# Performance work log

Hardware: AMD Instinct MI355X
Metric: run time of the kernel (lower is better)

Reference implementation:

```python
import jax, jax.numpy as jnp
import numpy as np

B, S, D, H, E, KW = 2, 2048, 1024, 8, 128, 16  # batch, seq, d_model, heads, head_width, kernel_width


def setup_inputs() -> dict:
    key = jax.random.key(0)
    ks = jax.random.split(key, 10)
    sc = D ** -0.5
    x = jax.random.normal(ks[0], (B, S, D), dtype=jnp.float32)
    Wq = jax.random.normal(ks[1], (H, D, E), dtype=jnp.float32) * sc
    bq = jnp.zeros((H, E), dtype=jnp.float32)
    Wk = jax.random.normal(ks[2], (H, D, E), dtype=jnp.float32) * sc
    bk = jnp.zeros((H, E), dtype=jnp.float32)
    Wv = jax.random.normal(ks[3], (H, D, E), dtype=jnp.float32) * sc
    bv = jnp.zeros((H, E), dtype=jnp.float32)
    Wo = jax.random.normal(ks[4], (H, E, D), dtype=jnp.float32) * ((H * E) ** -0.5)
    bo = jnp.zeros((D,), dtype=jnp.float32)
    dilations = jnp.array([1, 1, 2, 2, 4, 4, 8, 8], dtype=jnp.int32)
    return {"x": x, "Wq": Wq, "bq": bq, "Wk": Wk, "bk": bk,
            "Wv": Wv, "bv": bv, "Wo": Wo, "bo": bo, "dilations": dilations}


def _windows(kh, vh, bkh, bvh, d):
    # kh, vh: [B, S, E] projected keys/values for one head; d: dilation (scalar int)
    s = kh.shape[1]
    # center-justified dilated window: positions i + d*j - d*(KW-1)//2
    pos = jnp.arange(s)[:, None] + d * jnp.arange(KW)[None, :] - (d * (KW - 1)) // 2
    valid = (pos >= 0) & (pos < s)            # [S, KW]
    posc = jnp.clip(pos, 0, s - 1)
    # padded positions hold the zero-embedding, whose projection is just the bias
    kw = jnp.where(valid[None, :, :, None], kh[:, posc, :], bkh)  # [B, S, KW, E]
    vw = jnp.where(valid[None, :, :, None], vh[:, posc, :], bvh)
    return kw, vw


def _lcsa(x, Wq, bq, Wk, bk, Wv, bv, Wo, bo, dilations):
    # per-head independent projections (Core.Linear with parallel shape [heads])
    q = jnp.einsum('bsd,hde->bhse', x, Wq) + bq[None, :, None, :]       # [B,H,S,E]
    k_all = jnp.einsum('bsd,hde->bhse', x, Wk) + bk[None, :, None, :]
    v_all = jnp.einsum('bsd,hde->bhse', x, Wv) + bv[None, :, None, :]
    # gather dilated local windows per head (project-then-gather; padded = bias)
    kw, vw = jax.vmap(_windows, in_axes=(1, 1, 0, 0, 0))(k_all, v_all, bk, bv, dilations)
    # kw, vw: [H, B, S, KW, E]
    logits = jnp.einsum('bhse,hbske->bhsk', q, kw)                       # [B,H,S,KW]
    score = jax.nn.softmax(logits, axis=-1)
    # NOTE: original divides by sqrt(d_head) AFTER softmax*value (faithful quirk)
    attn = jnp.einsum('bhsk,hbske->bhse', score, vw) / jnp.sqrt(jnp.asarray(E, x.dtype))
    out = jnp.einsum('bhse,hed->bsd', attn, Wo) + bo                     # dehead merge
    return out


def reference(x, Wq, bq, Wk, bk, Wv, bv, Wo, bo, dilations):
    return _lcsa(x, Wq, bq, Wk, bk, Wv, bv, Wo, bo, dilations)
```

## Files before the change

### kernel.cpp

```cpp
#include <hip/hip_runtime.h>
#include <stdint.h>

#define Bb 2
#define Ss 2048
#define Dd 1024
#define Hh 8
#define Ee 128
#define KWW 16
#define Mm (Bb*Ss)
#define Kk 1024

typedef unsigned short u16;
typedef __attribute__((ext_vector_type(8))) _Float16 f16x8;
typedef __attribute__((ext_vector_type(4))) float f32x4;

__device__ __forceinline__ u16 f2h(float f) {
  union { _Float16 h; u16 u; } v; v.h = (_Float16)f; return v.u;
}
__device__ __forceinline__ float h2f(u16 u) {
  union { u16 u; _Float16 h; } v; v.u = u; return (float)v.h;
}
__device__ __forceinline__ float h2f_lo(uint32_t w) { return h2f((u16)(w & 0xFFFF)); }
__device__ __forceinline__ float h2f_hi(uint32_t w) { return h2f((u16)(w >> 16)); }

__device__ __forceinline__ void gll16(const void* g, void* l) {
  __builtin_amdgcn_global_load_lds((const __attribute__((address_space(1))) void*)g,
                                   (__attribute__((address_space(3))) void*)l, 16, 0, 0);
}

__global__ __launch_bounds__(256) void prep(
    const float* __restrict__ x, const float* __restrict__ Wq,
    const float* __restrict__ Wk, const float* __restrict__ Wv,
    const float* __restrict__ Wo,
    u16* __restrict__ xh, u16* __restrict__ wT, u16* __restrict__ woT) {
  const int bid = blockIdx.x;
  const int tid = threadIdx.x;
  if (bid < 4096) {
    int i = (bid * 256 + tid) * 4;
    float4 f = *(const float4*)(x + i);
    uint64_t pk = (uint64_t)f2h(f.x) | ((uint64_t)f2h(f.y) << 16) |
                  ((uint64_t)f2h(f.z) << 32) | ((uint64_t)f2h(f.w) << 48);
    *(uint64_t*)(xh + i) = pk;
    return;
  }
  __shared__ float tile[32][33];
  const int tx = tid & 31, ty = tid >> 5;
  if (bid < 4096 + 3072) {
    const int idx = bid - 4096;
    const int z = idx >> 7, rem = idx & 127;
    const int h = z & 7;
    const float* W = (z < 8) ? Wq : (z < 16) ? Wk : Wv;
    const float* ib = W + (size_t)h * Dd * Ee;
    u16* ob = wT + (size_t)z * Ee * Kk;
    const int r0 = (rem & 31) * 32, c0 = (rem >> 5) * 32;
    #pragma unroll
    for (int kq = 0; kq < 4; kq++)
      tile[ty + 8*kq][tx] = ib[(size_t)(r0 + ty + 8*kq) * Ee + (c0 + tx)];
    __syncthreads();
    #pragma unroll
    for (int kq = 0; kq < 4; kq++)
      ob[(size_t)(c0 + ty + 8*kq) * Dd + (r0 + tx)] = f2h(tile[tx][ty + 8*kq]);
  } else {
    const int idx = bid - (4096 + 3072);
    const int r0 = (idx & 31) * 32, c0 = (idx >> 5) * 32;
    const int R = Hh * Ee, C = Dd;
    #pragma unroll
    for (int kq = 0; kq < 4; kq++)
      tile[ty + 8*kq][tx] = Wo[(size_t)(r0 + ty + 8*kq) * C + (c0 + tx)];
    __syncthreads();
    #pragma unroll
    for (int kq = 0; kq < 4; kq++)
      woT[(size_t)(c0 + ty + 8*kq) * R + (r0 + tx)] = f2h(tile[tx][ty + 8*kq]);
  }
}

template<int MT>
__device__ __forceinline__ void gemm_core(
    const u16* __restrict__ A, const u16* __restrict__ Bt,
    u16* As, u16* Bs, f32x4 (&acc)[MT / 32][4]) {
  constexpr int MI = MT / 32;
  const int tid = threadIdx.x;
  const int wave = tid >> 6;
  const int lane = tid & 63;
  const size_t lnoff = (size_t)(lane >> 3) * Kk + (size_t)(((lane & 7) ^ (lane >> 3)) * 8);

  const int wm = (wave >> 1) * (MT / 2);
  const int wn = (wave & 1) * 64;
  const int fr = lane & 15;
  const int q  = lane >> 4;
  const int sw = fr & 7;

  #pragma unroll
  for (int i = 0; i < MI; i++)
    #pragma unroll
    for (int j = 0; j < 4; j++)
      #pragma unroll
      for (int r = 0; r < 4; r++) acc[i][j][r] = 0.0f;

  for (int kt = 0; kt < Kk; kt += 64) {
    #pragma unroll
    for (int c = 0; c < MI; c++)
      gll16(A + lnoff + (size_t)((c * 4 + wave) * 8) * Kk + kt, As + (c * 4 + wave) * 512);
    #pragma unroll
    for (int c = 0; c < 4; c++)
      gll16(Bt + lnoff + (size_t)((c * 4 + wave) * 8) * Kk + kt, Bs + (c * 4 + wave) * 512);
    __syncthreads();
    #pragma unroll
    for (int ks = 0; ks < 2; ks++) {
      const int col = ((ks << 2) | q) ^ sw;
      f16x8 ah[MI], bh[4];
      #pragma unroll
      for (int i = 0; i < MI; i++)
        ah[i] = *(const f16x8*)(As + (wm + i * 16 + fr) * 64 + col * 8);
      #pragma unroll
      for (int j = 0; j < 4; j++)
        bh[j] = *(const f16x8*)(Bs + (wn + j * 16 + fr) * 64 + col * 8);
      #pragma unroll
      for (int i = 0; i < MI; i++)
        #pragma unroll
        for (int j = 0; j < 4; j++)
          acc[i][j] = __builtin_amdgcn_mfma_f32_16x16x32_f16(ah[i], bh[j], acc[i][j], 0, 0, 0);
    }
    __syncthreads();
  }
}


__global__ __launch_bounds__(256) void gemm_qkv(
    const u16* __restrict__ xh, const u16* __restrict__ wT,
    const float* __restrict__ bq, const float* __restrict__ bk, const float* __restrict__ bv,
    u16* __restrict__ q, u16* __restrict__ k, u16* __restrict__ v) {
  __shared__ u16 As[128 * 64];
  __shared__ u16 Bs[128 * 64];
  const int m0 = blockIdx.x * 128;
  const int z = blockIdx.z;
  const int proj = z >> 3, h = z & 7;
  f32x4 acc[4][4];
  gemm_core<128>(xh + (size_t)m0 * Kk, wT + (size_t)z * (Ee * Kk), As, Bs, acc);

  u16* dst = proj == 0 ? q : (proj == 1 ? k : v);
  const float* bias = proj == 0 ? bq : (proj == 1 ? bk : bv);
  const int wave = threadIdx.x >> 6, lane = threadIdx.x & 63;
  const int wm = (wave >> 1) * 64, wn = (wave & 1) * 64;
  const int cn = lane & 15, rq4 = (lane >> 4) * 4;
  #pragma unroll
  for (int j = 0; j < 4; j++) {
    const int e = wn + j * 16 + cn;
    const float bb = bias[h * Ee + e];
    #pragma unroll
    for (int i = 0; i < 4; i++) {
      #pragma unroll
      for (int r = 0; r < 4; r++) {
        const int m = m0 + wm + i * 16 + rq4 + r;
        const int b = m >> 11, s = m & (Ss - 1);
        dst[(((size_t)(b * Hh + h)) * Ss + s) * Ee + e] = f2h(acc[i][j][r] + bb);
      }
    }
  }
}

__global__ __launch_bounds__(256) void gemm_out(
    const u16* __restrict__ attn, const u16* __restrict__ woT,
    const float* __restrict__ bo, float* __restrict__ out) {
  __shared__ u16 As[64 * 64];
  __shared__ u16 Bs[128 * 64];
  const int m0 = blockIdx.x * 64;
  const int n0 = blockIdx.y * 128;
  f32x4 acc[2][4];
  gemm_core<64>(attn + (size_t)m0 * Kk, woT + (size_t)n0 * Kk, As, Bs, acc);
  const int wave = threadIdx.x >> 6, lane = threadIdx.x & 63;
  const int wm = (wave >> 1) * 32, wn = (wave & 1) * 64;
  const int cn = lane & 15, rq4 = (lane >> 4) * 4;
  #pragma unroll
  for (int j = 0; j < 4; j++) {
    const int n = n0 + wn + j * 16 + cn;
    const float bb = bo[n];
    #pragma unroll
    for (int i = 0; i < 2; i++) {
      #pragma unroll
      for (int r = 0; r < 4; r++) {
        const int m = m0 + wm + i * 16 + rq4 + r;
        out[(size_t)m * Dd + n] = acc[i][j][r] + bb;
      }
    }
  }
}

__global__ __launch_bounds__(256) void attn_kernel(
    const u16* __restrict__ q, const u16* __restrict__ k, const u16* __restrict__ v,
    const float* __restrict__ bk, const float* __restrict__ bv,
    const int* __restrict__ dil, u16* __restrict__ attn) {
  const int nblk = (Bb * Hh * Ss) / 4;
  const int blk = (blockIdx.x & 7) * (nblk / 8) + (blockIdx.x >> 3);
  const int wid = blk * 4 + (threadIdx.x >> 6);
  const int lane = threadIdx.x & 63;
  const int s = wid & (Ss - 1);
  const int bh = wid >> 11;
  const int h = bh & 7, b = bh >> 3;
  const int d = dil[h];
  const size_t base = (size_t)bh * Ss * Ee;
  const u16* kp = k + base;
  const u16* vp = v + base;
  const uint32_t qw = *(const uint32_t*)(q + base + (size_t)s * Ee + 2 * lane);
  const float qx = h2f_lo(qw), qy = h2f_hi(qw);
  const float2 bk2 = ((const float2*)(bk + h * Ee))[lane];
  const float2 bv2 = ((const float2*)(bv + h * Ee))[lane];
  const int off = (d * (KWW - 1)) >> 1;
  const int J = (lane >> 2) & 15;

  float logit[KWW];
  #pragma unroll
  for (int j = 0; j < KWW; j++) {
    const int pos = s + d * j - off;
    if (pos >= 0 && pos < Ss) {
      uint32_t kw = *(const uint32_t*)(kp + (size_t)pos * Ee + 2 * lane);
      logit[j] = qx * h2f_lo(kw) + qy * h2f_hi(kw);
    } else {
      logit[j] = qx * bk2.x + qy * bk2.y;
    }
  }
  float vvx[KWW], vvy[KWW];
  #pragma unroll
  for (int t = 0; t < KWW; t++) {
    const int j = J ^ t;
    const int pos = s + d * j - off;
    const int posc = min(max(pos, 0), Ss - 1);
    uint32_t vw = *(const uint32_t*)(vp + (size_t)posc * Ee + 2 * lane);
    const bool ok = (pos >= 0) && (pos < Ss);
    vvx[t] = ok ? h2f_lo(vw) : bv2.x;
    vvy[t] = ok ? h2f_hi(vw) : bv2.y;
  }

  {
    const bool hi = (lane & 32) != 0;
    #pragma unroll
    for (int j = 0; j < 8; j++) {
      float send = hi ? logit[j] : logit[j + 8];
      float recv = __shfl_xor(send, 32, 64);
      logit[j] = (hi ? logit[j + 8] : logit[j]) + recv;
    }
  }
  {
    const bool hi = (lane & 16) != 0;
    #pragma unroll
    for (int j = 0; j < 4; j++) {
      float send = hi ? logit[j] : logit[j + 4];
      float recv = __shfl_xor(send, 16, 64);
      logit[j] = (hi ? logit[j + 4] : logit[j]) + recv;
    }
  }
  {
    const bool hi = (lane & 8) != 0;
    #pragma unroll
    for (int j = 0; j < 2; j++) {
      float send = hi ? logit[j] : logit[j + 2];
      float recv = __shfl_xor(send, 8, 64);
      logit[j] = (hi ? logit[j + 2] : logit[j]) + recv;
    }
  }
  float own;
  {
    const bool hi = (lane & 4) != 0;
    float send = hi ? logit[0] : logit[1];
    float recv = __shfl_xor(send, 4, 64);
    own = (hi ? logit[1] : logit[0]) + recv;
  }
  own += __shfl_xor(own, 2, 64);
  own += __shfl_xor(own, 1, 64);

  float mx = own;
  mx = fmaxf(mx, __shfl_xor(mx, 4, 64));
  mx = fmaxf(mx, __shfl_xor(mx, 8, 64));
  mx = fmaxf(mx, __shfl_xor(mx, 16, 64));
  mx = fmaxf(mx, __shfl_xor(mx, 32, 64));
  float w = __expf(own - mx);
  float sum = w;
  sum += __shfl_xor(sum, 4, 64);
  sum += __shfl_xor(sum, 8, 64);
  sum += __shfl_xor(sum, 16, 64);
  sum += __shfl_xor(sum, 32, 64);
  w *= 1.0f / (sum * 11.313708498984760f);

  float g[KWW];
  g[0] = w;
  g[1] = __shfl_xor(g[0], 4, 64);
  #pragma unroll
  for (int t = 0; t < 2; t++) g[2 + t] = __shfl_xor(g[t], 8, 64);
  #pragma unroll
  for (int t = 0; t < 4; t++) g[4 + t] = __shfl_xor(g[t], 16, 64);
  #pragma unroll
  for (int t = 0; t < 8; t++) g[8 + t] = __shfl_xor(g[t], 32, 64);

  float ax = 0.f, ay = 0.f;
  #pragma unroll
  for (int t = 0; t < KWW; t++) { ax += g[t] * vvx[t]; ay += g[t] * vvy[t]; }

  u16* op = attn + ((size_t)(b * Ss + s)) * (Hh * Ee) + h * Ee + 2 * lane;
  *(uint32_t*)op = (uint32_t)f2h(ax) | ((uint32_t)f2h(ay) << 16);
}

extern "C" void kernel_launch(void* const* d_in, const int* in_sizes, int n_in,
                              void* d_out, int out_size, void* d_ws, size_t ws_size,
                              hipStream_t stream) {
  (void)in_sizes; (void)n_in; (void)out_size; (void)ws_size;
  const float* x  = (const float*)d_in[0];
  const float* Wq = (const float*)d_in[1];
  const float* bq = (const float*)d_in[2];
  const float* Wk = (const float*)d_in[3];
  const float* bk = (const float*)d_in[4];
  const float* Wv = (const float*)d_in[5];
  const float* bv = (const float*)d_in[6];
  const float* Wo = (const float*)d_in[7];
  const float* bo = (const float*)d_in[8];
  const int* dil  = (const int*)d_in[9];
  float* out = (float*)d_out;

  char* ws = (char*)d_ws;
  u16* xh  = (u16*)ws;  ws += (size_t)Mm * Kk * 2;
  u16* wT  = (u16*)ws;  ws += (size_t)24 * Ee * Kk * 2;
  u16* woT = (u16*)ws;  ws += (size_t)Kk * Dd * 2;
  u16* q = (u16*)ws; ws += (size_t)Bb * Hh * Ss * Ee * 2;
  u16* k = (u16*)ws; ws += (size_t)Bb * Hh * Ss * Ee * 2;
  u16* v = (u16*)ws; ws += (size_t)Bb * Hh * Ss * Ee * 2;
  u16* attn = xh;

  prep<<<8192, 256, 0, stream>>>(x, Wq, Wk, Wv, Wo, xh, wT, woT);
  gemm_qkv<<<dim3(Mm / 128, 1, 24), 256, 0, stream>>>(xh, wT, bq, bk, bv, q, k, v);
  attn_kernel<<<(Bb * Hh * Ss) / 4, 256, 0, stream>>>(q, k, v, bk, bv, dil, attn);
  gemm_out<<<dim3(Mm / 64, Dd / 128), 256, 0, stream>>>(attn, woT, bo, out);
}
```

Measured before the change: 181.2 us.

## Pre-swizzle weights into MFMA fragment layout and load B directly to registers

The weight transpose/convert step now writes Wq/Wk/Wv/Wo in a fragment-major layout (k/8, n, k%8) so each lane can fetch its MFMA B operand with one 16-byte global load. The GEMM core drops the shared-memory B tile and instead register-prefetches the next k-step's B fragments while computing the current one. This removes the LDS traffic and LDS footprint for B, at the cost of more vector registers and redundant global/L2 reads of B across waves.

```diff
diff --git a/kernel.cpp b/kernel.cpp
--- a/kernel.cpp
+++ b/kernel.cpp
@@ -57,27 +57,34 @@
     for (int kq = 0; kq < 4; kq++)
       tile[ty + 8*kq][tx] = ib[(size_t)(r0 + ty + 8*kq) * Ee + (c0 + tx)];
     __syncthreads();
-    #pragma unroll
-    for (int kq = 0; kq < 4; kq++)
-      ob[(size_t)(c0 + ty + 8*kq) * Dd + (r0 + tx)] = f2h(tile[tx][ty + 8*kq]);
+    const int k = r0 + tx;
+    #pragma unroll
+    for (int kq = 0; kq < 4; kq++) {
+      const int n = c0 + ty + 8*kq;
+      ob[(((size_t)(k >> 3) * 128 + n) << 3) + (k & 7)] = f2h(tile[tx][ty + 8*kq]);
+    }
   } else {
     const int idx = bid - (4096 + 3072);
     const int r0 = (idx & 31) * 32, c0 = (idx >> 5) * 32;
-    const int R = Hh * Ee, C = Dd;
+    const int C = Dd;
     #pragma unroll
     for (int kq = 0; kq < 4; kq++)
       tile[ty + 8*kq][tx] = Wo[(size_t)(r0 + ty + 8*kq) * C + (c0 + tx)];
     __syncthreads();
-    #pragma unroll
-    for (int kq = 0; kq < 4; kq++)
-      woT[(size_t)(c0 + ty + 8*kq) * R + (r0 + tx)] = f2h(tile[tx][ty + 8*kq]);
+    const int k = r0 + tx;
+    #pragma unroll
+    for (int kq = 0; kq < 4; kq++) {
+      const int n = c0 + ty + 8*kq;
+      woT[(size_t)(n >> 7) * 131072 +
+          (((size_t)(k >> 3) * 128 + (n & 127)) << 3) + (k & 7)] = f2h(tile[tx][ty + 8*kq]);
+    }
   }
 }
 
 template<int MT>
 __device__ __forceinline__ void gemm_core(
-    const u16* __restrict__ A, const u16* __restrict__ Bt,
-    u16* As, u16* Bs, f32x4 (&acc)[MT / 32][4]) {
+    const u16* __restrict__ A, const u16* __restrict__ Btf,
+    u16* As, f32x4 (&acc)[MT / 32][4]) {
   constexpr int MI = MT / 32;
   const int tid = threadIdx.x;
   const int wave = tid >> 6;
@@ -90,6 +97,14 @@
   const int q  = lane >> 4;
   const int sw = fr & 7;
 
+  const u16* bptr = Btf + ((size_t)q * 128 + wn + fr) * 8;
+  f16x8 bcur[8], bnxt[8];
+  #pragma unroll
+  for (int ks = 0; ks < 2; ks++)
+    #pragma unroll
+    for (int j = 0; j < 4; j++)
+      bcur[ks * 4 + j] = *(const f16x8*)(bptr + (ks * 4) * 1024 + j * 128);
+
   #pragma unroll
   for (int i = 0; i < MI; i++)
     #pragma unroll
@@ -101,27 +116,29 @@
     #pragma unroll
     for (int c = 0; c < MI; c++)
       gll16(A + lnoff + (size_t)((c * 4 + wave) * 8) * Kk + kt, As + (c * 4 + wave) * 512);
-    #pragma unroll
-    for (int c = 0; c < 4; c++)
-      gll16(Bt + lnoff + (size_t)((c * 4 + wave) * 8) * Kk + kt, Bs + (c * 4 + wave) * 512);
     __syncthreads();
+    const int ktn = (kt + 64) & (Kk - 1);
+    #pragma unroll
+    for (int ks = 0; ks < 2; ks++)
+      #pragma unroll
+      for (int j = 0; j < 4; j++)
+        bnxt[ks * 4 + j] = *(const f16x8*)(bptr + ((ktn >> 3) + ks * 4) * 1024 + j * 128);
     #pragma unroll
     for (int ks = 0; ks < 2; ks++) {
       const int col = ((ks << 2) | q) ^ sw;
-      f16x8 ah[MI], bh[4];
+      f16x8 ah[MI];
       #pragma unroll
       for (int i = 0; i < MI; i++)
         ah[i] = *(const f16x8*)(As + (wm + i * 16 + fr) * 64 + col * 8);
-      #pragma unroll
-      for (int j = 0; j < 4; j++)
-        bh[j] = *(const f16x8*)(Bs + (wn + j * 16 + fr) * 64 + col * 8);
       #pragma unroll
       for (int i = 0; i < MI; i++)
         #pragma unroll
         for (int j = 0; j < 4; j++)
-          acc[i][j] = __builtin_amdgcn_mfma_f32_16x16x32_f16(ah[i], bh[j], acc[i][j], 0, 0, 0);
+          acc[i][j] = __builtin_amdgcn_mfma_f32_16x16x32_f16(ah[i], bcur[ks * 4 + j], acc[i][j], 0, 0, 0);
     }
     __syncthreads();
+    #pragma unroll
+    for (int t = 0; t < 8; t++) bcur[t] = bnxt[t];
   }
 }
 
@@ -131,12 +148,11 @@
     const float* __restrict__ bq, const float* __restrict__ bk, const float* __restrict__ bv,
     u16* __restrict__ q, u16* __restrict__ k, u16* __restrict__ v) {
   __shared__ u16 As[128 * 64];
-  __shared__ u16 Bs[128 * 64];
   const int m0 = blockIdx.x * 128;
   const int z = blockIdx.z;
   const int proj = z >> 3, h = z & 7;
   f32x4 acc[4][4];
-  gemm_core<128>(xh + (size_t)m0 * Kk, wT + (size_t)z * (Ee * Kk), As, Bs, acc);
+  gemm_core<128>(xh + (size_t)m0 * Kk, wT + (size_t)z * (Ee * Kk), As, acc);
 
   u16* dst = proj == 0 ? q : (proj == 1 ? k : v);
   const float* bias = proj == 0 ? bq : (proj == 1 ? bk : bv);
@@ -163,11 +179,10 @@
     const u16* __restrict__ attn, const u16* __restrict__ woT,
     const float* __restrict__ bo, float* __restrict__ out) {
   __shared__ u16 As[64 * 64];
-  __shared__ u16 Bs[128 * 64];
   const int m0 = blockIdx.x * 64;
   const int n0 = blockIdx.y * 128;
   f32x4 acc[2][4];
-  gemm_core<64>(attn + (size_t)m0 * Kk, woT + (size_t)n0 * Kk, As, Bs, acc);
+  gemm_core<64>(attn + (size_t)m0 * Kk, woT + (size_t)blockIdx.y * 131072, As, acc);
   const int wave = threadIdx.x >> 6, lane = threadIdx.x & 63;
   const int wm = (wave >> 1) * 32, wn = (wave & 1) * 64;
   const int cn = lane & 15, rq4 = (lane >> 4) * 4;
```

After: 178.9 us. About the same (-1.3%).
